# Performance work log

Hardware: AMD Instinct MI355X
Metric: run time of the kernel (lower is better)

Reference implementation:

```python
import jax, jax.numpy as jnp
import numpy as np

N = 16384   # total gate nodes (64 graphs x 256 gates)
B = 64      # graphs in batch
E = 49152   # directed edges (avg in-degree 3)
Q = 32      # qubit_num
F = 256     # feat_dim
D = 2 * F   # node feature dim = 512
H = 2       # heads
A = 128     # action_num


def _gatv2(x, wl, wr, att, b, src, dst, n):
    # PyG GATv2Conv (concat=True, share_weights=False, negative_slope=0.2)
    h, c = att.shape
    xl = (x @ wl).reshape(n, h, c)   # source-side projection [N,H,C]
    xr = (x @ wr).reshape(n, h, c)   # target-side projection [N,H,C]
    e = jax.nn.leaky_relu(xl[src] + xr[dst], 0.2)       # [E,H,C]
    logit = jnp.einsum('ehc,hc->eh', e, att)             # [E,H]
    m = jax.ops.segment_max(logit, dst, num_segments=n)  # softmax over in-edges per target
    p = jnp.exp(logit - m[dst])
    den = jax.ops.segment_sum(p, dst, num_segments=n)
    alpha = p / den[dst]                                 # [E,H]
    out = jax.ops.segment_sum(alpha[:, :, None] * xl[src], dst, num_segments=n)
    return out.reshape(n, h * c) + b


def _forward(x, xt_w1, xt_b1, xt_w2, xt_b2,
             g0_wl, g0_wr, g0_att, g0_b,
             g1_wl, g1_wr, g1_att, g1_b,
             g2_wl, g2_wr, g2_att, g2_b,
             g3_wl, g3_wr, g3_att, g3_b,
             g4_wl, g4_wr, g4_att, g4_b,
             ln_w, ln_b, aggr_t,
             m_w1, m_b1, m_w2, m_b2, m_w3, m_b3,
             edge_index, batch):
    lr = lambda v: jax.nn.leaky_relu(v, 0.01)
    # x_trans: Linear -> LeakyReLU -> Linear, then fold qubit-pairs into one node
    h0 = lr(x @ xt_w1 + xt_b1) @ xt_w2 + xt_b2           # [2N, F]
    cx = h0.reshape(-1, D)                               # [N, 2F]
    n = cx.shape[0]
    # GATv2Conv default add_self_loops=True (inputs contain no self loops)
    sl = jnp.arange(n, dtype=edge_index.dtype)
    src = jnp.concatenate([edge_index[0], sl])
    dst = jnp.concatenate([edge_index[1], sl])
    res = cx
    h = lr(_gatv2(cx, g0_wl, g0_wr, g0_att, g0_b, src, dst, n))
    for wl_, wr_, att_, b_ in ((g1_wl, g1_wr, g1_att, g1_b),
                               (g2_wl, g2_wr, g2_att, g2_b),
                               (g3_wl, g3_wr, g3_att, g3_b)):
        h = lr(_gatv2(h, wl_, wr_, att_, b_, src, dst, n))
    h = lr(_gatv2(h, g4_wl, g4_wr, g4_att, g4_b, src, dst, n))
    h = h + res                                           # residual [N, 2F]
    # PyG LayerNorm(mode='graph'): normalize over nodes AND channels per graph
    cnt = jax.ops.segment_sum(jnp.ones((n,), h.dtype), batch, num_segments=B)
    norm = cnt * h.shape[1]
    mean = jax.ops.segment_sum(h.sum(-1), batch, num_segments=B) / norm
    hc = h - mean[batch][:, None]
    var = jax.ops.segment_sum((hc * hc).sum(-1), batch, num_segments=B) / norm
    h = hc / jnp.sqrt(var + 1e-5)[batch][:, None] * ln_w + ln_b
    # SoftmaxAggregation(learn=True): channel-wise softmax over nodes per graph
    logit = h * aggr_t
    mg = jax.ops.segment_max(logit, batch, num_segments=B)
    p = jnp.exp(logit - mg[batch])
    den = jax.ops.segment_sum(p, batch, num_segments=B)
    g = jax.ops.segment_sum((p / den[batch]) * h, batch, num_segments=B)  # [B, 2F]
    # head MLP 512->384->256->128
    o = lr(g @ m_w1 + m_b1)
    o = lr(o @ m_w2 + m_b2)
    return o @ m_w3 + m_b3


def setup_inputs() -> dict:
    key = jax.random.key(0)
    ks = iter(jax.random.split(key, 64))
    def rn(shp, s=0.05):
        return jax.random.normal(next(ks), shp, jnp.float32) * s
    d = {}
    d['x'] = jax.random.normal(next(ks), (2 * N, Q), jnp.float32)
    src = jax.random.randint(next(ks), (E,), 0, N, jnp.int32)
    off = jax.random.randint(next(ks), (E,), 1, N, jnp.int32)
    d['edge_index'] = jnp.stack([src, (src + off) % N])  # no self loops
    d['batch'] = jnp.arange(N, dtype=jnp.int32) // (N // B)
    d['xt_w1'] = rn((Q, F)); d['xt_b1'] = rn((F,))
    d['xt_w2'] = rn((F, F)); d['xt_b2'] = rn((F,))
    d['g0_wl'] = rn((D, H * D)); d['g0_wr'] = rn((D, H * D))
    d['g0_att'] = rn((H, D));    d['g0_b'] = rn((H * D,))
    for i in (1, 2, 3):
        d[f'g{i}_wl'] = rn((H * D, H * D)); d[f'g{i}_wr'] = rn((H * D, H * D))
        d[f'g{i}_att'] = rn((H, D));        d[f'g{i}_b'] = rn((H * D,))
    d['g4_wl'] = rn((H * D, D)); d['g4_wr'] = rn((H * D, D))
    d['g4_att'] = rn((1, D));    d['g4_b'] = rn((D,))
    d['ln_w'] = jnp.ones((D,), jnp.float32); d['ln_b'] = jnp.zeros((D,), jnp.float32)
    d['aggr_t'] = jnp.array(1.0, jnp.float32)
    d['m_w1'] = rn((D, 384)); d['m_b1'] = rn((384,))
    d['m_w2'] = rn((384, 256)); d['m_b2'] = rn((256,))
    d['m_w3'] = rn((256, A)); d['m_b3'] = rn((A,))
    return d


def reference(x, edge_index, batch, xt_w1, xt_b1, xt_w2, xt_b2,
              g0_wl, g0_wr, g0_att, g0_b,
              g1_wl, g1_wr, g1_att, g1_b,
              g2_wl, g2_wr, g2_att, g2_b,
              g3_wl, g3_wr, g3_att, g3_b,
              g4_wl, g4_wr, g4_att, g4_b,
              ln_w, ln_b, aggr_t,
              m_w1, m_b1, m_w2, m_b2, m_w3, m_b3):
    return _forward(x, xt_w1, xt_b1, xt_w2, xt_b2,
                    g0_wl, g0_wr, g0_att, g0_b,
                    g1_wl, g1_wr, g1_att, g1_b,
                    g2_wl, g2_wr, g2_att, g2_b,
                    g3_wl, g3_wr, g3_att, g3_b,
                    g4_wl, g4_wr, g4_att, g4_b,
                    ln_w, ln_b, aggr_t,
                    m_w1, m_b1, m_w2, m_b2, m_w3, m_b3,
                    edge_index, batch)
```

## Files before the change

### kernel.cpp

```cpp
#include <hip/hip_runtime.h>
#include <hip/hip_bf16.h>

typedef __hip_bfloat16 bf16;

#define NN 16384
#define BBG 64
#define EE 49152
#define ET (EE + NN)
#define DD 512
#define NG (NN / BBG)

__device__ __forceinline__ float b2f(bf16 v) { return __bfloat162float(v); }
__device__ __forceinline__ bf16 f2b(float v) { return __float2bfloat16(v); }
__device__ __forceinline__ float sb2f(short s) {
    unsigned u = ((unsigned)(unsigned short)s) << 16;
    return __builtin_bit_cast(float, u);
}
__device__ __forceinline__ short f2bs(float v) {
    bf16 b = f2b(v);
    return __builtin_bit_cast(short, b);
}
__device__ __forceinline__ int clampi(int v, int lo, int hi)
{
    return v < lo ? lo : (v > hi ? hi : v);
}

typedef __attribute__((ext_vector_type(8))) short bf16x8;
typedef __attribute__((ext_vector_type(4))) float f32x4;

#define AS1 __attribute__((address_space(1)))
#define AS3 __attribute__((address_space(3)))

__global__ __launch_bounds__(256) void gemm_mfma_bt(
    const bf16* __restrict__ A, const bf16* __restrict__ Bt,
    const float* __restrict__ bias, float* __restrict__ C,
    bf16* __restrict__ Cb, int M, int N, int K, float slope, int has_act)
{
    __shared__ bf16 As[128 * 32];
    __shared__ bf16 Bs[128 * 32];
    const int tid = threadIdx.x;
    const int w = tid >> 6;
    const int l = tid & 63;
    const int bm = blockIdx.y * 128;
    const int bn = blockIdx.x * 128;
    const int wrow = (w >> 1) * 64;
    const int wcol = (w & 1) * 64;
    const int quad = l >> 4;
    const int c16 = l & 15;

    const int lrow = l >> 2;
    const int lchunk = l & 3;
    const bf16* Ag = A + (size_t)(bm + w * 16 + lrow) * K + lchunk * 8;
    const bf16* Bg = Bt + (size_t)(bn + w * 16 + lrow) * K + lchunk * 8;
    char* AsB = (char*)As;
    char* BsB = (char*)Bs;

    f32x4 acc[4][4] = {};

    for (int k0 = 0; k0 < K; k0 += 32) {
        __builtin_amdgcn_global_load_lds((const AS1 void*)(Ag + k0),
            (AS3 void*)(AsB + w * 1024), 16, 0, 0);
        __builtin_amdgcn_global_load_lds((const AS1 void*)(Ag + (size_t)64 * K + k0),
            (AS3 void*)(AsB + 4096 + w * 1024), 16, 0, 0);
        __builtin_amdgcn_global_load_lds((const AS1 void*)(Bg + k0),
            (AS3 void*)(BsB + w * 1024), 16, 0, 0);
        __builtin_amdgcn_global_load_lds((const AS1 void*)(Bg + (size_t)64 * K + k0),
            (AS3 void*)(BsB + 4096 + w * 1024), 16, 0, 0);
        __syncthreads();

        bf16x8 a[4], b[4];
#pragma unroll
        for (int i = 0; i < 4; i++) {
            int ra = wrow + i * 16 + c16;
            a[i] = *(const bf16x8*)(AsB + ra * 64 + quad * 16);
            int rb = wcol + i * 16 + c16;
            b[i] = *(const bf16x8*)(BsB + rb * 64 + quad * 16);
        }
#pragma unroll
        for (int i = 0; i < 4; i++)
#pragma unroll
            for (int j = 0; j < 4; j++)
                acc[i][j] = __builtin_amdgcn_mfma_f32_16x16x32_bf16(
                    a[i], b[j], acc[i][j], 0, 0, 0);
        __syncthreads();
    }

#pragma unroll
    for (int i = 0; i < 4; i++) {
#pragma unroll
        for (int j = 0; j < 4; j++) {
            int col = bn + wcol + j * 16 + c16;
            float bv = bias ? bias[col] : 0.f;
#pragma unroll
            for (int r = 0; r < 4; r++) {
                int row = bm + wrow + i * 16 + quad * 4 + r;
                float v = acc[i][j][r] + bv;
                if (has_act) v = (v >= 0.f) ? v : v * slope;
                if (C)  C[(size_t)row * N + col] = v;
                if (Cb) Cb[(size_t)row * N + col] = f2b(v);
            }
        }
    }
}

__global__ __launch_bounds__(256) void gemm_mfma_dual(
    const bf16* __restrict__ A, const bf16* __restrict__ Bt,
    bf16* __restrict__ X0, bf16* __restrict__ X1,
    int M, int Ntot, int K, int HC)
{
    __shared__ bf16 As[128 * 32];
    __shared__ bf16 Bs[128 * 32];
    const int tid = threadIdx.x;
    const int w = tid >> 6;
    const int l = tid & 63;
    const int bm = blockIdx.y * 128;
    const int bn = blockIdx.x * 128;
    const int wrow = (w >> 1) * 64;
    const int wcol = (w & 1) * 64;
    const int quad = l >> 4;
    const int c16 = l & 15;

    const int lrow = l >> 2;
    const int lchunk = l & 3;
    const bf16* Ag = A + (size_t)(bm + w * 16 + lrow) * K + lchunk * 8;
    const bf16* Bg = Bt + (size_t)(bn + w * 16 + lrow) * K + lchunk * 8;
    char* AsB = (char*)As;
    char* BsB = (char*)Bs;

    f32x4 acc[4][4] = {};

    for (int k0 = 0; k0 < K; k0 += 32) {
        __builtin_amdgcn_global_load_lds((const AS1 void*)(Ag + k0),
            (AS3 void*)(AsB + w * 1024), 16, 0, 0);
        __builtin_amdgcn_global_load_lds((const AS1 void*)(Ag + (size_t)64 * K + k0),
            (AS3 void*)(AsB + 4096 + w * 1024), 16, 0, 0);
        __builtin_amdgcn_global_load_lds((const AS1 void*)(Bg + k0),
            (AS3 void*)(BsB + w * 1024), 16, 0, 0);
        __builtin_amdgcn_global_load_lds((const AS1 void*)(Bg + (size_t)64 * K + k0),
            (AS3 void*)(BsB + 4096 + w * 1024), 16, 0, 0);
        __syncthreads();

        bf16x8 a[4], b[4];
#pragma unroll
        for (int i = 0; i < 4; i++) {
            int ra = wrow + i * 16 + c16;
            a[i] = *(const bf16x8*)(AsB + ra * 64 + quad * 16);
            int rb = wcol + i * 16 + c16;
            b[i] = *(const bf16x8*)(BsB + rb * 64 + quad * 16);
        }
#pragma unroll
        for (int i = 0; i < 4; i++)
#pragma unroll
            for (int j = 0; j < 4; j++)
                acc[i][j] = __builtin_amdgcn_mfma_f32_16x16x32_bf16(
                    a[i], b[j], acc[i][j], 0, 0, 0);
        __syncthreads();
    }

#pragma unroll
    for (int i = 0; i < 4; i++) {
#pragma unroll
        for (int j = 0; j < 4; j++) {
            int col = bn + wcol + j * 16 + c16;
            bf16* dst = (col < HC) ? (X0 + col) : (X1 + col - HC);
#pragma unroll
            for (int r = 0; r < 4; r++) {
                int row = bm + wrow + i * 16 + quad * 4 + r;
                dst[(size_t)row * HC] = f2b(acc[i][j][r]);
            }
        }
    }
}

__global__ __launch_bounds__(256) void gemm_f32(
    const float* __restrict__ A, const float* __restrict__ W,
    const float* __restrict__ bias, float* __restrict__ C,
    int M, int N, int K, float slope, int has_act)
{
    const int BK = 16;
    __shared__ float Asm[BK][64 + 1];
    __shared__ float Wsm[BK][64 + 1];
    int tid = threadIdx.x;
    int bm = blockIdx.y * 64;
    int bn = blockIdx.x * 64;
    int tr = tid >> 4;
    int tc = tid & 15;
    float acc[4][4] = {};

    for (int k0 = 0; k0 < K; k0 += BK) {
        {
            int col = tid & 15;
            int row = tid >> 4;
#pragma unroll
            for (int p = 0; p < 4; p++) {
                int r = row + p * 16;
                Asm[col][r] = A[(size_t)(bm + r) * K + k0 + col];
            }
        }
        {
            int wc = tid & 63;
            int wr = tid >> 6;
#pragma unroll
            for (int p = 0; p < 4; p++) {
                int r = wr + p * 4;
                Wsm[r][wc] = W[(size_t)(k0 + r) * N + bn + wc];
            }
        }
        __syncthreads();
#pragma unroll
        for (int kk = 0; kk < BK; kk++) {
            float a[4], w[4];
#pragma unroll
            for (int i = 0; i < 4; i++) a[i] = Asm[kk][tr * 4 + i];
#pragma unroll
            for (int j = 0; j < 4; j++) w[j] = Wsm[kk][tc * 4 + j];
#pragma unroll
            for (int i = 0; i < 4; i++)
#pragma unroll
                for (int j = 0; j < 4; j++)
                    acc[i][j] += a[i] * w[j];
        }
        __syncthreads();
    }
#pragma unroll
    for (int i = 0; i < 4; i++) {
        int r = bm + tr * 4 + i;
#pragma unroll
        for (int j = 0; j < 4; j++) {
            int cn = bn + tc * 4 + j;
            float v = acc[i][j];
            if (bias) v += bias[cn];
            if (has_act) v = (v >= 0.f) ? v : v * slope;
            C[(size_t)r * N + cn] = v;
        }
    }
}

__global__ __launch_bounds__(256) void transpose_f2b2(
    const float* __restrict__ in0, bf16* __restrict__ out0,
    const float* __restrict__ in1, bf16* __restrict__ out1, int R, int C)
{
    const float* in = blockIdx.z ? in1 : in0;
    bf16* out = blockIdx.z ? out1 : out0;
    __shared__ float tile[32][33];
    int c0 = blockIdx.x * 32;
    int r0 = blockIdx.y * 32;
    int tx = threadIdx.x & 31;
    int ty = threadIdx.x >> 5;
#pragma unroll
    for (int k = 0; k < 4; k++) {
        int r = ty + k * 8;
        tile[r][tx] = in[(size_t)(r0 + r) * C + c0 + tx];
    }
    __syncthreads();
#pragma unroll
    for (int k = 0; k < 4; k++) {
        int rr = ty + k * 8;
        out[(size_t)(c0 + rr) * R + r0 + tx] = f2b(tile[tx][rr]);
    }
}

__global__ void f2b_vec(const float* __restrict__ in, bf16* __restrict__ out, int n)
{
    int i = blockIdx.x * 256 + threadIdx.x;
    if (i < n) out[i] = f2b(in[i]);
}

__global__ void count_deg(const int* __restrict__ ei, int* __restrict__ deg)
{
    int e = blockIdx.x * 256 + threadIdx.x;
    if (e >= ET) return;
    int d = (e < EE) ? ei[EE + e] : (e - EE);
    d = clampi(d, 0, NN - 1);
    atomicAdd(&deg[d], 1);
}

__global__ __launch_bounds__(256) void scan_deg(const int* __restrict__ deg,
                                                int* __restrict__ rs)
{
    __shared__ int part[256];
    __shared__ int psum[257];
    int tid = threadIdx.x;
    const int per = NN / 256;
    int base = tid * per;
    int s = 0;
    for (int i = 0; i < per; i++) s += deg[base + i];
    part[tid] = s;
    __syncthreads();
    if (tid == 0) {
        int acc = 0;
        for (int i = 0; i < 256; i++) { psum[i] = acc; acc += part[i]; }
        psum[256] = acc;
    }
    __syncthreads();
    int acc = psum[tid];
    for (int i = 0; i < per; i++) { rs[base + i] = acc; acc += deg[base + i]; }
    if (tid == 0) rs[NN] = psum[256];
}

__global__ void fill_csr(const int* __restrict__ ei, const int* __restrict__ rs,
                         int* __restrict__ cur, int* __restrict__ csrc)
{
    int e = blockIdx.x * 256 + threadIdx.x;
    if (e >= ET) return;
    int s, d;
    if (e < EE) { s = ei[e]; d = ei[EE + e]; } else { s = d = e - EE; }
    s = clampi(s, 0, NN - 1);
    d = clampi(d, 0, NN - 1);
    int pos = atomicAdd(&cur[d], 1);
    int slot = clampi(rs[d] + pos, 0, ET - 1);
    csrc[slot] = s;
}

template<int NH>
__global__ __launch_bounds__(256) void gat_wave7(
    const bf16* __restrict__ xl, const bf16* __restrict__ xr,
    const float* __restrict__ att, const float* __restrict__ bias,
    const int* __restrict__ rs, const int* __restrict__ csrc,
    const float* __restrict__ res, float* __restrict__ out_f,
    bf16* __restrict__ out_b, float* __restrict__ lnsums)
{
    constexpr int HC = NH * 512;
    constexpr int PF = 6;
    constexpr int NODES = (NH == 2) ? 8 : 4;
    constexpr int WPB = (NH == 2) ? 4 : 2;
    constexpr int SLOTS = (NH == 2) ? 7 : 9;
    __shared__ char smem[WPB * 2 * SLOTS * 1024];

    const int tid = threadIdx.x;
    const int w = tid >> 6;
    const int lane = tid & 63;
    const int wave_id = blockIdx.x * WPB + w;

    int msrc[NODES];
    int sdeg[NODES];
#pragma unroll
    for (int it = 0; it < NODES; ++it) {
        int gw = wave_id * NODES + it;
        int n = (NH == 2) ? (gw >> 1) : gw;
        int st = rs[n];
        int deg = clampi(rs[n + 1] - st, 1, 64);
        st = clampi(st, 0, ET - 1);
        st = __builtin_amdgcn_readfirstlane(st);
        deg = __builtin_amdgcn_readfirstlane(deg);
        sdeg[it] = deg;
        msrc[it] = csrc[st + ((lane < deg) ? lane : deg - 1)];
    }

    float av0[8], av1[8], bv0[8], bv1[8];
    {
        f32x4 t0 = *(const f32x4*)(att + lane * 8);
        f32x4 t1 = *(const f32x4*)(att + lane * 8 + 4);
        f32x4 u0 = *(const f32x4*)(bias + lane * 8);
        f32x4 u1 = *(const f32x4*)(bias + lane * 8 + 4);
#pragma unroll
        for (int k = 0; k < 4; k++) {
            av0[k] = t0[k]; av0[4 + k] = t1[k];
            bv0[k] = u0[k]; bv0[4 + k] = u1[k];
        }
        if (NH == 2) {
            f32x4 t2 = *(const f32x4*)(att + 512 + lane * 8);
            f32x4 t3 = *(const f32x4*)(att + 512 + lane * 8 + 4);
            f32x4 u2 = *(const f32x4*)(bias + 512 + lane * 8);
            f32x4 u3 = *(const f32x4*)(bias + 512 + lane * 8 + 4);
#pragma unroll
            for (int k = 0; k < 4; k++) {
                av1[k] = t2[k]; av1[4 + k] = t3[k];
                bv1[k] = u2[k]; bv1[4 + k] = u3[k];
            }
        } else {
#pragma unroll
            for (int k = 0; k < 8; k++) { av1[k] = av0[k]; bv1[k] = bv0[k]; }
        }
    }

    auto issue = [&](int it, int pb) {
        int gw = wave_id * NODES + it;
        int n = (NH == 2) ? (gw >> 1) : gw;
        int h = (NH == 2) ? (gw & 1) : 0;
        char* buf = smem + (size_t)((w * 2 + pb) * SLOTS) * 1024;
        const bf16* xrrow = xr + (size_t)n * HC + h * 512 + lane * 8;
        __builtin_amdgcn_global_load_lds((const AS1 void*)xrrow,
            (AS3 void*)buf, 16, 0, 0);
        int dm1 = sdeg[it] - 1;
#pragma unroll
        for (int r = 0; r < PF; r++) {
            int idx = (r < dm1) ? r : dm1;
            int s = __builtin_amdgcn_readlane(msrc[it], idx);
            s = clampi(s, 0, NN - 1);
            const bf16* row = xl + (size_t)s * HC + h * 512 + lane * 8;
            __builtin_amdgcn_global_load_lds((const AS1 void*)row,
                (AS3 void*)(buf + (1 + r) * 1024), 16, 0, 0);
        }
        if (NH == 1) {
            const float* rr = res + (size_t)n * 512 + lane * 4;
            __builtin_amdgcn_global_load_lds((const AS1 void*)rr,
                (AS3 void*)(buf + 7 * 1024), 16, 0, 0);
            __builtin_amdgcn_global_load_lds((const AS1 void*)(rr + 256),
                (AS3 void*)(buf + 8 * 1024), 16, 0, 0);
        }
    };

    auto compute = [&](int it, int pb) {
        int gw = wave_id * NODES + it;
        int n = (NH == 2) ? (gw >> 1) : gw;
        int h = (NH == 2) ? (gw & 1) : 0;
        int cb = h * 512 + lane * 8;
        int deg = sdeg[it];
        char* buf = smem + (size_t)((w * 2 + pb) * SLOTS) * 1024;

        float rv[8], av[8];
        {
            bf16x8 xb = *(const bf16x8*)(buf + lane * 16);
#pragma unroll
            for (int k = 0; k < 8; k++) {
                rv[k] = sb2f(xb[k]);
                av[k] = h ? av1[k] : av0[k];
            }
        }
        bf16x8 rloc[PF];
#pragma unroll
        for (int r = 0; r < PF; r++)
            rloc[r] = *(const bf16x8*)(buf + (1 + r) * 1024 + lane * 16);

        float part[PF];
#pragma unroll
        for (int r = 0; r < PF; r++) {
            float p0 = 0.f, p1 = 0.f, p2 = 0.f, p3 = 0.f;
#pragma unroll
            for (int k = 0; k < 8; k += 4) {
                float x0 = sb2f(rloc[r][k + 0]);
                float x1 = sb2f(rloc[r][k + 1]);
                float x2 = sb2f(rloc[r][k + 2]);
                float x3 = sb2f(rloc[r][k + 3]);
                float u0 = x0 + rv[k + 0]; u0 = (u0 >= 0.f) ? u0 : 0.2f * u0;
                float u1 = x1 + rv[k + 1]; u1 = (u1 >= 0.f) ? u1 : 0.2f * u1;
                float u2 = x2 + rv[k + 2]; u2 = (u2 >= 0.f) ? u2 : 0.2f * u2;
                float u3 = x3 + rv[k + 3]; u3 = (u3 >= 0.f) ? u3 : 0.2f * u3;
                p0 = fmaf(av[k + 0], u0, p0);
                p1 = fmaf(av[k + 1], u1, p1);
                p2 = fmaf(av[k + 2], u2, p2);
                p3 = fmaf(av[k + 3], u3, p3);
            }
            part[r] = (p0 + p1) + (p2 + p3);
        }

#pragma unroll
        for (int msk = 32; msk; msk >>= 1) {
#pragma unroll
            for (int r = 0; r < PF; r++) part[r] += __shfl_xor(part[r], msk);
        }

        float m = -1e30f;
#pragma unroll
        for (int r = 0; r < PF; r++) {
            float vr = (r < deg) ? part[r] : -1e30f;
            m = fmaxf(m, vr);
        }
        float den = 0.f;
        float pw[PF];
#pragma unroll
        for (int r = 0; r < PF; r++) {
            float e = __expf(part[r] - m);
            pw[r] = (r < deg) ? e : 0.f;
            den += pw[r];
        }

        float acc[8];
#pragma unroll
        for (int k = 0; k < 8; k++) acc[k] = 0.f;
#pragma unroll
        for (int r = 0; r < PF; r++) {
#pragma unroll
            for (int k = 0; k < 8; k++)
                acc[k] = fmaf(pw[r], sb2f(rloc[r][k]), acc[k]);
        }

        if (deg > PF) {
            for (int i = PF; i < deg; i++) {
                int s = __builtin_amdgcn_readlane(msrc[it], i);
                s = clampi(s, 0, NN - 1);
                f32x4 rw = *(const f32x4*)(xl + (size_t)s * HC + cb);
                bf16x8 rb = __builtin_bit_cast(bf16x8, rw);
                float pt = 0.f;
#pragma unroll
                for (int k = 0; k < 8; k++) {
                    float x = sb2f(rb[k]);
                    float u = x + rv[k];
                    u = (u >= 0.f) ? u : 0.2f * u;
                    pt = fmaf(av[k], u, pt);
                }
#pragma unroll
                for (int msk = 32; msk; msk >>= 1) pt += __shfl_xor(pt, msk);
                float mn = fmaxf(m, pt);
                float rr = __expf(m - mn);
                float pi = __expf(pt - mn);
                m = mn;
                den = den * rr + pi;
#pragma unroll
                for (int k = 0; k < 8; k++) {
                    float x = sb2f(rb[k]);
                    acc[k] = fmaf(acc[k], rr, pi * x);
                }
            }
        }

        float inv = 1.f / den;
        float vals[8];
#pragma unroll
        for (int k = 0; k < 8; k++) {
            float bv = h ? bv1[k] : bv0[k];
            float v = fmaf(acc[k], inv, bv);
            v = (v >= 0.f) ? v : 0.01f * v;
            vals[k] = v;
        }
        if (NH == 1) {
            f32x4 r0 = *(const f32x4*)(buf + 7 * 1024 + lane * 32);
            f32x4 r1 = *(const f32x4*)(buf + 7 * 1024 + lane * 32 + 16);
            float ls = 0.f, ls2 = 0.f;
#pragma unroll
            for (int k = 0; k < 8; k++) {
                vals[k] += (k < 4) ? r0[k] : r1[k - 4];
                ls += vals[k];
                ls2 += vals[k] * vals[k];
            }
#pragma unroll
            for (int v = 0; v < 2; v++) {
                f32x4 ov;
#pragma unroll
                for (int k = 0; k < 4; k++) ov[k] = vals[v * 4 + k];
                *(f32x4*)(out_f + (size_t)n * HC + cb + v * 4) = ov;
            }
#pragma unroll
            for (int msk = 32; msk; msk >>= 1) {
                ls += __shfl_xor(ls, msk);
                ls2 += __shfl_xor(ls2, msk);
            }
            if (lane == 0) {
                int g = n >> 8;
                atomicAdd(&lnsums[g], ls);
                atomicAdd(&lnsums[BBG + g], ls2);
            }
        } else {
            bf16x8 ov;
#pragma unroll
            for (int k = 0; k < 8; k++) ov[k] = f2bs(vals[k]);
            *(bf16x8*)(out_b + (size_t)n * HC + cb) = ov;
        }
    };

    issue(0, 0);
#pragma unroll
    for (int it = 0; it < NODES; ++it) {
        int pb = it & 1;
        if (it + 1 < NODES) {
            issue(it + 1, pb ^ 1);
            if (NH == 2) asm volatile("s_waitcnt vmcnt(7)" ::: "memory");
            else         asm volatile("s_waitcnt vmcnt(9)" ::: "memory");
        } else {
            asm volatile("s_waitcnt vmcnt(0)" ::: "memory");
        }
        __builtin_amdgcn_sched_barrier(0);
        compute(it, pb);
    }
}

__global__ __launch_bounds__(256) void aggr_partial(
    const float* __restrict__ h, const float* __restrict__ lnsums,
    const float* __restrict__ lnw, const float* __restrict__ lnb,
    const float* __restrict__ t_, float* __restrict__ pm,
    float* __restrict__ pd, float* __restrict__ pa)
{
    int g = blockIdx.x, ch = blockIdx.y, nk = blockIdx.z;
    int tid = threadIdx.x;
    int c = ch * 256 + tid;
    const float tot = (float)(NG * DD);
    float S = lnsums[g], S2 = lnsums[BBG + g];
    float mu = S / tot;
    float iv = rsqrtf(fmaxf(S2 / tot - mu * mu, 0.f) + 1e-5f);
    float w = lnw[c], b = lnb[c], t = t_[0];
    size_t base = (size_t)g * NG * DD + (size_t)nk * 32 * DD + c;
    float m = -1e30f, den = 0.f, acc = 0.f;
    for (int i = 0; i < 32; i++) {
        float hn = (h[base + (size_t)i * DD] - mu) * iv * w + b;
        float lg = hn * t;
        if (lg > m) {
            float r = __expf(m - lg);
            den *= r; acc *= r; m = lg;
        }
        float p = __expf(lg - m);
        den += p; acc += p * hn;
    }
    size_t idx = (((size_t)g * 2 + ch) * 8 + nk) * 256 + tid;
    pm[idx] = m; pd[idx] = den; pa[idx] = acc;
}

__global__ __launch_bounds__(256) void aggr_combine(
    const float* __restrict__ pm, const float* __restrict__ pd,
    const float* __restrict__ pa, float* __restrict__ gout)
{
    int g = blockIdx.x, ch = blockIdx.y;
    int tid = threadIdx.x;
    size_t base = (((size_t)g * 2 + ch) * 8) * 256 + tid;
    float m = -1e30f;
#pragma unroll
    for (int k = 0; k < 8; k++) m = fmaxf(m, pm[base + k * 256]);
    float den = 0.f, acc = 0.f;
#pragma unroll
    for (int k = 0; k < 8; k++) {
        float r = __expf(pm[base + k * 256] - m);
        den += pd[base + k * 256] * r;
        acc += pa[base + k * 256] * r;
    }
    gout[(size_t)g * DD + ch * 256 + tid] = acc / den;
}

extern "C" void kernel_launch(void* const* d_in, const int* in_sizes, int n_in,
                              void* d_out, int out_size, void* d_ws, size_t ws_size,
                              hipStream_t stream)
{
    const float* x      = (const float*)d_in[0];
    const int*   ei     = (const int*)d_in[1];
    const float* xt_w1  = (const float*)d_in[3];
    const float* xt_b1  = (const float*)d_in[4];
    const float* xt_w2  = (const float*)d_in[5];
    const float* xt_b2  = (const float*)d_in[6];
    const float* ln_w   = (const float*)d_in[27];
    const float* ln_b   = (const float*)d_in[28];
    const float* aggr_t = (const float*)d_in[29];
    const float* m_w1   = (const float*)d_in[30];
    const float* m_b1   = (const float*)d_in[31];
    const float* m_w2   = (const float*)d_in[32];
    const float* m_b2   = (const float*)d_in[33];
    const float* m_w3   = (const float*)d_in[34];
    const float* m_b3   = (const float*)d_in[35];
    float* out = (float*)d_out;

    char* p = (char*)d_ws;
    auto take = [&](size_t bytes) {
        char* r = p;
        p += (bytes + 255) & ~(size_t)255;
        return r;
    };
    int* i_deg     = (int*)take((size_t)(NN + 1) * 4);
    int* i_rs      = (int*)take((size_t)(NN + 1) * 4);
    int* i_cur     = (int*)take((size_t)NN * 4);
    int* i_src     = (int*)take((size_t)ET * 4);
    float* f_sums  = (float*)take((size_t)2 * BBG * 4);
    float* f_pm    = (float*)take((size_t)BBG * 2 * 8 * 256 * 4);
    float* f_pd    = (float*)take((size_t)BBG * 2 * 8 * 256 * 4);
    float* f_pa    = (float*)take((size_t)BBG * 2 * 8 * 256 * 4);
    float* b_g     = (float*)take((size_t)BBG * DD * 4);
    float* b_m1    = (float*)take((size_t)BBG * 384 * 4);
    float* b_m2    = (float*)take((size_t)BBG * 256 * 4);
    float* b_res   = (float*)take((size_t)NN * DD * 4);
    float* b_h     = (float*)take((size_t)NN * DD * 4);
    bf16* b_resb   = (bf16*)take((size_t)NN * DD * 2);
    bf16* b_hb     = (bf16*)take((size_t)NN * 1024 * 2);
    bf16* b_xlb    = (bf16*)take((size_t)NN * 1024 * 2);
    bf16* b_xrb    = (bf16*)take((size_t)NN * 1024 * 2);
    bf16* b_xb     = (bf16*)take((size_t)2 * NN * 32 * 2);
    bf16* b_wcat   = (bf16*)take((size_t)2048 * 1024 * 2);
    bf16* b_w1b    = (bf16*)take((size_t)32 * 256 * 2);
    bf16* b_w2b    = (bf16*)take((size_t)256 * 256 * 2);
    bf16* b_t1b = b_hb;

    dim3 blk(256);

    hipMemsetAsync(i_deg, 0, (size_t)(NN + 1) * 4, stream);
    hipMemsetAsync(i_cur, 0, (size_t)NN * 4, stream);
    hipMemsetAsync(f_sums, 0, (size_t)2 * BBG * 4, stream);
    count_deg<<<ET / 256, blk, 0, stream>>>(ei, i_deg);
    scan_deg<<<1, blk, 0, stream>>>(i_deg, i_rs);
    fill_csr<<<ET / 256, blk, 0, stream>>>(ei, i_rs, i_cur, i_src);

    f2b_vec<<<(2 * NN * 32 + 255) / 256, blk, 0, stream>>>(x, b_xb, 2 * NN * 32);
    transpose_f2b2<<<dim3(256 / 32, 32 / 32, 1), blk, 0, stream>>>(
        xt_w1, b_w1b, xt_w1, b_w1b, 32, 256);
    transpose_f2b2<<<dim3(256 / 32, 256 / 32, 1), blk, 0, stream>>>(
        xt_w2, b_w2b, xt_w2, b_w2b, 256, 256);

    gemm_mfma_bt<<<dim3(256 / 128, 32768 / 128), blk, 0, stream>>>(
        b_xb, b_w1b, xt_b1, (float*)nullptr, b_t1b, 32768, 256, 32, 0.01f, 1);
    gemm_mfma_bt<<<dim3(256 / 128, 32768 / 128), blk, 0, stream>>>(
        b_t1b, b_w2b, xt_b2, b_res, b_resb, 32768, 256, 256, 0.f, 0);

    for (int L = 0; L < 5; L++) {
        const float* wl  = (const float*)d_in[7 + 4 * L];
        const float* wr  = (const float*)d_in[8 + 4 * L];
        const float* att = (const float*)d_in[9 + 4 * L];
        const float* gb  = (const float*)d_in[10 + 4 * L];
        int Fin = (L == 0) ? 512 : 1024;
        int HC  = (L == 4) ? 512 : 1024;
        const bf16* hin = (L == 0) ? b_resb : b_hb;

        transpose_f2b2<<<dim3(HC / 32, Fin / 32, 2), blk, 0, stream>>>(
            wl, b_wcat, wr, b_wcat + (size_t)HC * Fin, Fin, HC);
        gemm_mfma_dual<<<dim3(2 * HC / 128, NN / 128), blk, 0, stream>>>(
            hin, b_wcat, b_xlb, b_xrb, NN, 2 * HC, Fin, HC);
        if (L == 4) {
            gat_wave7<1><<<2048, dim3(128), 0, stream>>>(
                b_xlb, b_xrb, att, gb, i_rs, i_src,
                b_res, b_h, (bf16*)nullptr, f_sums);
        } else {
            gat_wave7<2><<<1024, blk, 0, stream>>>(
                b_xlb, b_xrb, att, gb, i_rs, i_src,
                (const float*)nullptr, (float*)nullptr, b_hb, (float*)nullptr);
        }
    }

    aggr_partial<<<dim3(BBG, 2, 8), blk, 0, stream>>>(
        b_h, f_sums, ln_w, ln_b, aggr_t, f_pm, f_pd, f_pa);
    aggr_combine<<<dim3(BBG, 2), blk, 0, stream>>>(f_pm, f_pd, f_pa, b_g);

    gemm_f32<<<dim3(384 / 64, 1), blk, 0, stream>>>(
        b_g, m_w1, m_b1, b_m1, 64, 384, 512, 0.01f, 1);
    gemm_f32<<<dim3(256 / 64, 1), blk, 0, stream>>>(
        b_m1, m_w2, m_b2, b_m2, 64, 256, 384, 0.01f, 1);
    gemm_f32<<<dim3(128 / 64, 1), blk, 0, stream>>>(
        b_m2, m_w3, m_b3, out, 64, 128, 256, 0.f, 0);
}
```

Before: 1.048 ms.

## Use 256x256 double-buffered MFMA GEMM and register-prefetch GAT kernel for last layer

Replaces the 128x128 dual-projection GEMM with a templated 256x256 tile kernel using 512 threads, K-step 64, and double-buffered LDS staging via global_load_lds with explicit waitcnt and barriers, plus s_setprio around MFMA bursts. The aim is more data reuse per loaded tile and overlap of loads with compute. The final single-head GAT layer now uses a new kernel that prefetches neighbour rows into registers instead of LDS, with 4 waves per block. The trade-off is 128KB of LDS per block, so only one block fits per CU, and a larger register footprint.

```diff
diff --git a/kernel.cpp b/kernel.cpp
--- a/kernel.cpp
+++ b/kernel.cpp
@@ -103,69 +103,115 @@
     }
 }
 
-__global__ __launch_bounds__(256) void gemm_mfma_dual(
+template<int KK>
+__global__ __launch_bounds__(512, 1) void gemm256_dual(
     const bf16* __restrict__ A, const bf16* __restrict__ Bt,
-    bf16* __restrict__ X0, bf16* __restrict__ X1,
-    int M, int Ntot, int K, int HC)
-{
-    __shared__ bf16 As[128 * 32];
-    __shared__ bf16 Bs[128 * 32];
+    bf16* __restrict__ X0, bf16* __restrict__ X1, int HC)
+{
+    constexpr int NT = KK / 64;
+    __shared__ char smem[131072];
+    char* const Abuf[2] = { smem,         smem + 65536 };
+    char* const Bbuf[2] = { smem + 32768, smem + 98304 };
     const int tid = threadIdx.x;
     const int w = tid >> 6;
     const int l = tid & 63;
-    const int bm = blockIdx.y * 128;
-    const int bn = blockIdx.x * 128;
-    const int wrow = (w >> 1) * 64;
-    const int wcol = (w & 1) * 64;
+    const int wm = w >> 2;
+    const int wn = w & 3;
     const int quad = l >> 4;
     const int c16 = l & 15;
-
-    const int lrow = l >> 2;
-    const int lchunk = l & 3;
-    const bf16* Ag = A + (size_t)(bm + w * 16 + lrow) * K + lchunk * 8;
-    const bf16* Bg = Bt + (size_t)(bn + w * 16 + lrow) * K + lchunk * 8;
-    char* AsB = (char*)As;
-    char* BsB = (char*)Bs;
-
-    f32x4 acc[4][4] = {};
-
-    for (int k0 = 0; k0 < K; k0 += 32) {
-        __builtin_amdgcn_global_load_lds((const AS1 void*)(Ag + k0),
-            (AS3 void*)(AsB + w * 1024), 16, 0, 0);
-        __builtin_amdgcn_global_load_lds((const AS1 void*)(Ag + (size_t)64 * K + k0),
-            (AS3 void*)(AsB + 4096 + w * 1024), 16, 0, 0);
-        __builtin_amdgcn_global_load_lds((const AS1 void*)(Bg + k0),
-            (AS3 void*)(BsB + w * 1024), 16, 0, 0);
-        __builtin_amdgcn_global_load_lds((const AS1 void*)(Bg + (size_t)64 * K + k0),
-            (AS3 void*)(BsB + 4096 + w * 1024), 16, 0, 0);
-        __syncthreads();
-
-        bf16x8 a[4], b[4];
-#pragma unroll
-        for (int i = 0; i < 4; i++) {
-            int ra = wrow + i * 16 + c16;
-            a[i] = *(const bf16x8*)(AsB + ra * 64 + quad * 16);
-            int rb = wcol + i * 16 + c16;
-            b[i] = *(const bf16x8*)(BsB + rb * 64 + quad * 16);
-        }
-#pragma unroll
-        for (int i = 0; i < 4; i++)
-#pragma unroll
-            for (int j = 0; j < 4; j++)
-                acc[i][j] = __builtin_amdgcn_mfma_f32_16x16x32_bf16(
-                    a[i], b[j], acc[i][j], 0, 0, 0);
-        __syncthreads();
-    }
-
-#pragma unroll
-    for (int i = 0; i < 4; i++) {
-#pragma unroll
-        for (int j = 0; j < 4; j++) {
-            int col = bn + wcol + j * 16 + c16;
+    const int bm = blockIdx.y * 256;
+    const int bn = blockIdx.x * 256;
+
+    const int srow = w * 32 + (l >> 3);
+    const int schunk = (l & 7) * 8;
+    const bf16* AgS = A + (size_t)(bm + srow) * KK + schunk;
+    const bf16* BgS = Bt + (size_t)(bn + srow) * KK + schunk;
+    const int lbase = (w * 32) * 128;
+
+    auto stage = [&](int k0, int buf) {
+#pragma unroll
+        for (int op = 0; op < 4; ++op)
+            __builtin_amdgcn_global_load_lds(
+                (const AS1 void*)(AgS + (size_t)(op * 8) * KK + k0),
+                (AS3 void*)(Abuf[buf] + lbase + op * 1024), 16, 0, 0);
+#pragma unroll
+        for (int op = 0; op < 4; ++op)
+            __builtin_amdgcn_global_load_lds(
+                (const AS1 void*)(BgS + (size_t)(op * 8) * KK + k0),
+                (AS3 void*)(Bbuf[buf] + lbase + op * 1024), 16, 0, 0);
+    };
+
+    f32x4 acc[8][4] = {};
+
+    auto tile_compute = [&](int buf) {
+        bf16x8 bfrag[4][2];
+#pragma unroll
+        for (int j = 0; j < 4; ++j)
+#pragma unroll
+            for (int ks = 0; ks < 2; ++ks) {
+                int rb = wn * 64 + j * 16 + c16;
+                bfrag[j][ks] = *(const bf16x8*)(Bbuf[buf] + rb * 128 + ks * 64 + quad * 16);
+            }
+#pragma unroll
+        for (int ip = 0; ip < 4; ++ip) {
+            bf16x8 afrag[2][2];
+#pragma unroll
+            for (int ii = 0; ii < 2; ++ii)
+#pragma unroll
+                for (int ks = 0; ks < 2; ++ks) {
+                    int ra = wm * 128 + (ip * 2 + ii) * 16 + c16;
+                    afrag[ii][ks] = *(const bf16x8*)(Abuf[buf] + ra * 128 + ks * 64 + quad * 16);
+                }
+            __builtin_amdgcn_s_setprio(1);
+#pragma unroll
+            for (int ii = 0; ii < 2; ++ii)
+#pragma unroll
+                for (int j = 0; j < 4; ++j)
+#pragma unroll
+                    for (int ks = 0; ks < 2; ++ks)
+                        acc[ip * 2 + ii][j] = __builtin_amdgcn_mfma_f32_16x16x32_bf16(
+                            afrag[ii][ks], bfrag[j][ks], acc[ip * 2 + ii][j], 0, 0, 0);
+            __builtin_amdgcn_s_setprio(0);
+        }
+    };
+
+    stage(0, 0);
+    stage(64, 1);
+    asm volatile("s_waitcnt vmcnt(8)" ::: "memory");
+    __builtin_amdgcn_s_barrier();
+
+#pragma unroll 1
+    for (int tp = 0; tp < NT / 2; ++tp) {
+        const int t0 = 2 * tp;
+        tile_compute(0);
+        __builtin_amdgcn_s_barrier();
+        if (t0 + 2 < NT) {
+            stage((t0 + 2) * 64, 0);
+            asm volatile("s_waitcnt vmcnt(8)" ::: "memory");
+        } else {
+            asm volatile("s_waitcnt vmcnt(0)" ::: "memory");
+        }
+        __builtin_amdgcn_s_barrier();
+        tile_compute(1);
+        __builtin_amdgcn_s_barrier();
+        if (t0 + 3 < NT) {
+            stage((t0 + 3) * 64, 1);
+            asm volatile("s_waitcnt vmcnt(8)" ::: "memory");
+        } else {
+            asm volatile("s_waitcnt vmcnt(0)" ::: "memory");
+        }
+        __builtin_amdgcn_s_barrier();
+    }
+
+#pragma unroll
+    for (int i = 0; i < 8; ++i) {
+#pragma unroll
+        for (int j = 0; j < 4; ++j) {
+            int col = bn + wn * 64 + j * 16 + c16;
             bf16* dst = (col < HC) ? (X0 + col) : (X1 + col - HC);
 #pragma unroll
-            for (int r = 0; r < 4; r++) {
-                int row = bm + wrow + i * 16 + quad * 4 + r;
+            for (int r = 0; r < 4; ++r) {
+                int row = bm + wm * 128 + i * 16 + quad * 4 + r;
                 dst[(size_t)row * HC] = f2b(acc[i][j][r]);
             }
         }
@@ -313,7 +359,7 @@
 }
 
 template<int NH>
-__global__ __launch_bounds__(256) void gat_wave7(
+__global__ __launch_bounds__(256, 4) void gat_wave6(
     const bf16* __restrict__ xl, const bf16* __restrict__ xr,
     const float* __restrict__ att, const float* __restrict__ bias,
     const int* __restrict__ rs, const int* __restrict__ csrc,
@@ -323,14 +369,10 @@
     constexpr int HC = NH * 512;
     constexpr int PF = 6;
     constexpr int NODES = (NH == 2) ? 8 : 4;
-    constexpr int WPB = (NH == 2) ? 4 : 2;
-    constexpr int SLOTS = (NH == 2) ? 7 : 9;
-    __shared__ char smem[WPB * 2 * SLOTS * 1024];
-
     const int tid = threadIdx.x;
     const int w = tid >> 6;
     const int lane = tid & 63;
-    const int wave_id = blockIdx.x * WPB + w;
+    const int wave_id = blockIdx.x * 4 + w;
 
     int msrc[NODES];
     int sdeg[NODES];
@@ -347,6 +389,233 @@
         msrc[it] = csrc[st + ((lane < deg) ? lane : deg - 1)];
     }
 
+    float av0[8], av1[8];
+    {
+        f32x4 t0 = *(const f32x4*)(att + lane * 8);
+        f32x4 t1 = *(const f32x4*)(att + lane * 8 + 4);
+#pragma unroll
+        for (int k = 0; k < 4; k++) { av0[k] = t0[k]; av0[4 + k] = t1[k]; }
+        if (NH == 2) {
+            f32x4 t2 = *(const f32x4*)(att + 512 + lane * 8);
+            f32x4 t3 = *(const f32x4*)(att + 512 + lane * 8 + 4);
+#pragma unroll
+            for (int k = 0; k < 4; k++) { av1[k] = t2[k]; av1[4 + k] = t3[k]; }
+        } else {
+#pragma unroll
+            for (int k = 0; k < 8; k++) av1[k] = av0[k];
+        }
+    }
+
+    f32x4 rows[2][PF];
+    f32x4 rpx[2];
+
+    auto issue = [&](int it, int pb) {
+        int gw = wave_id * NODES + it;
+        int n = (NH == 2) ? (gw >> 1) : gw;
+        int h = (NH == 2) ? (gw & 1) : 0;
+        int cb = h * 512 + lane * 8;
+        rpx[pb] = *(const f32x4*)(xr + (size_t)n * HC + cb);
+        int dm1 = sdeg[it] - 1;
+#pragma unroll
+        for (int r = 0; r < PF; r++) {
+            int idx = (r < dm1) ? r : dm1;
+            int s = __builtin_amdgcn_readlane(msrc[it], idx);
+            s = clampi(s, 0, NN - 1);
+            rows[pb][r] = *(const f32x4*)(xl + (size_t)s * HC + cb);
+        }
+    };
+
+    auto compute = [&](int it, int pb) {
+        int gw = wave_id * NODES + it;
+        int n = (NH == 2) ? (gw >> 1) : gw;
+        int h = (NH == 2) ? (gw & 1) : 0;
+        int cb = h * 512 + lane * 8;
+        int deg = sdeg[it];
+
+        float rv[8], av[8];
+        {
+            bf16x8 xb = __builtin_bit_cast(bf16x8, rpx[pb]);
+#pragma unroll
+            for (int k = 0; k < 8; k++) {
+                rv[k] = sb2f(xb[k]);
+                av[k] = h ? av1[k] : av0[k];
+            }
+        }
+
+        float part[PF];
+#pragma unroll
+        for (int r = 0; r < PF; r++) {
+            bf16x8 rb = __builtin_bit_cast(bf16x8, rows[pb][r]);
+            float p0 = 0.f, p1 = 0.f, p2 = 0.f, p3 = 0.f;
+#pragma unroll
+            for (int k = 0; k < 8; k += 4) {
+                float x0 = sb2f(rb[k + 0]);
+                float x1 = sb2f(rb[k + 1]);
+                float x2 = sb2f(rb[k + 2]);
+                float x3 = sb2f(rb[k + 3]);
+                float u0 = x0 + rv[k + 0]; u0 = (u0 >= 0.f) ? u0 : 0.2f * u0;
+                float u1 = x1 + rv[k + 1]; u1 = (u1 >= 0.f) ? u1 : 0.2f * u1;
+                float u2 = x2 + rv[k + 2]; u2 = (u2 >= 0.f) ? u2 : 0.2f * u2;
+                float u3 = x3 + rv[k + 3]; u3 = (u3 >= 0.f) ? u3 : 0.2f * u3;
+                p0 = fmaf(av[k + 0], u0, p0);
+                p1 = fmaf(av[k + 1], u1, p1);
+                p2 = fmaf(av[k + 2], u2, p2);
+                p3 = fmaf(av[k + 3], u3, p3);
+            }
+            part[r] = (p0 + p1) + (p2 + p3);
+        }
+
+#pragma unroll
+        for (int msk = 32; msk; msk >>= 1) {
+#pragma unroll
+            for (int r = 0; r < PF; r++) part[r] += __shfl_xor(part[r], msk);
+        }
+
+        float m = -1e30f;
+#pragma unroll
+        for (int r = 0; r < PF; r++) {
+            float vr = (r < deg) ? part[r] : -1e30f;
+            m = fmaxf(m, vr);
+        }
+        float den = 0.f;
+        float pw[PF];
+#pragma unroll
+        for (int r = 0; r < PF; r++) {
+            float e = __expf(part[r] - m);
+            pw[r] = (r < deg) ? e : 0.f;
+            den += pw[r];
+        }
+
+        float acc[8];
+#pragma unroll
+        for (int k = 0; k < 8; k++) acc[k] = 0.f;
+#pragma unroll
+        for (int r = 0; r < PF; r++) {
+            bf16x8 rb = __builtin_bit_cast(bf16x8, rows[pb][r]);
+#pragma unroll
+            for (int k = 0; k < 8; k++)
+                acc[k] = fmaf(pw[r], sb2f(rb[k]), acc[k]);
+        }
+
+        if (deg > PF) {
+            for (int i = PF; i < deg; i++) {
+                int s = __builtin_amdgcn_readlane(msrc[it], i);
+                s = clampi(s, 0, NN - 1);
+                f32x4 rw = *(const f32x4*)(xl + (size_t)s * HC + cb);
+                bf16x8 rb = __builtin_bit_cast(bf16x8, rw);
+                float pt = 0.f;
+#pragma unroll
+                for (int k = 0; k < 8; k++) {
+                    float x = sb2f(rb[k]);
+                    float u = x + rv[k];
+                    u = (u >= 0.f) ? u : 0.2f * u;
+                    pt = fmaf(av[k], u, pt);
+                }
+#pragma unroll
+                for (int msk = 32; msk; msk >>= 1) pt += __shfl_xor(pt, msk);
+                float mn = fmaxf(m, pt);
+                float rr = __expf(m - mn);
+                float pi = __expf(pt - mn);
+                m = mn;
+                den = den * rr + pi;
+#pragma unroll
+                for (int k = 0; k < 8; k++) {
+                    float x = sb2f(rb[k]);
+                    acc[k] = fmaf(acc[k], rr, pi * x);
+                }
+            }
+        }
+
+        float inv = 1.f / den;
+        f32x4 b0 = *(const f32x4*)(bias + cb);
+        f32x4 b1 = *(const f32x4*)(bias + cb + 4);
+        float vals[8];
+#pragma unroll
+        for (int k = 0; k < 8; k++) {
+            float bv = (k < 4) ? b0[k] : b1[k - 4];
+            float v = fmaf(acc[k], inv, bv);
+            v = (v >= 0.f) ? v : 0.01f * v;
+            vals[k] = v;
+        }
+        if (res) {
+            float ls = 0.f, ls2 = 0.f;
+#pragma unroll
+            for (int k = 0; k < 8; k++) {
+                vals[k] += res[(size_t)n * HC + cb + k];
+                ls += vals[k];
+                ls2 += vals[k] * vals[k];
+            }
+#pragma unroll
+            for (int v = 0; v < 2; v++) {
+                f32x4 ov;
+#pragma unroll
+                for (int k = 0; k < 4; k++) ov[k] = vals[v * 4 + k];
+                *(f32x4*)(out_f + (size_t)n * HC + cb + v * 4) = ov;
+            }
+            if (lnsums) {
+#pragma unroll
+                for (int msk = 32; msk; msk >>= 1) {
+                    ls += __shfl_xor(ls, msk);
+                    ls2 += __shfl_xor(ls2, msk);
+                }
+                if (lane == 0) {
+                    int g = n >> 8;
+                    atomicAdd(&lnsums[g], ls);
+                    atomicAdd(&lnsums[BBG + g], ls2);
+                }
+            }
+        } else {
+            bf16x8 ov;
+#pragma unroll
+            for (int k = 0; k < 8; k++) ov[k] = f2bs(vals[k]);
+            *(bf16x8*)(out_b + (size_t)n * HC + cb) = ov;
+        }
+    };
+
+    issue(0, 0);
+#pragma unroll
+    for (int it = 0; it < NODES; ++it) {
+        int pb = it & 1;
+        if (it + 1 < NODES) issue(it + 1, pb ^ 1);
+        compute(it, pb);
+    }
+}
+
+template<int NH>
+__global__ __launch_bounds__(256) void gat_wave7(
+    const bf16* __restrict__ xl, const bf16* __restrict__ xr,
+    const float* __restrict__ att, const float* __restrict__ bias,
+    const int* __restrict__ rs, const int* __restrict__ csrc,
+    const float* __restrict__ res, float* __restrict__ out_f,
+    bf16* __restrict__ out_b, float* __restrict__ lnsums)
+{
+    constexpr int HC = NH * 512;
+    constexpr int PF = 6;
+    constexpr int NODES = (NH == 2) ? 8 : 4;
+    constexpr int WPB = 4;
+    constexpr int SLOTS = 7;
+    __shared__ char smem[WPB * 2 * SLOTS * 1024];
+
+    const int tid = threadIdx.x;
+    const int w = tid >> 6;
+    const int lane = tid & 63;
+    const int wave_id = blockIdx.x * WPB + w;
+
+    int msrc[NODES];
+    int sdeg[NODES];
+#pragma unroll
+    for (int it = 0; it < NODES; ++it) {
+        int gw = wave_id * NODES + it;
+        int n = (NH == 2) ? (gw >> 1) : gw;
+        int st = rs[n];
+        int deg = clampi(rs[n + 1] - st, 1, 64);
+        st = clampi(st, 0, ET - 1);
+        st = __builtin_amdgcn_readfirstlane(st);
+        deg = __builtin_amdgcn_readfirstlane(deg);
+        sdeg[it] = deg;
+        msrc[it] = csrc[st + ((lane < deg) ? lane : deg - 1)];
+    }
+
     float av0[8], av1[8], bv0[8], bv1[8];
     {
         f32x4 t0 = *(const f32x4*)(att + lane * 8);
@@ -391,13 +660,6 @@
             const bf16* row = xl + (size_t)s * HC + h * 512 + lane * 8;
             __builtin_amdgcn_global_load_lds((const AS1 void*)row,
                 (AS3 void*)(buf + (1 + r) * 1024), 16, 0, 0);
-        }
-        if (NH == 1) {
-            const float* rr = res + (size_t)n * 512 + lane * 4;
-            __builtin_amdgcn_global_load_lds((const AS1 void*)rr,
-                (AS3 void*)(buf + 7 * 1024), 16, 0, 0);
-            __builtin_amdgcn_global_load_lds((const AS1 void*)(rr + 256),
-                (AS3 void*)(buf + 8 * 1024), 16, 0, 0);
         }
     };
 
@@ -514,39 +776,10 @@
             v = (v >= 0.f) ? v : 0.01f * v;
             vals[k] = v;
         }
-        if (NH == 1) {
-            f32x4 r0 = *(const f32x4*)(buf + 7 * 1024 + lane * 32);
-            f32x4 r1 = *(const f32x4*)(buf + 7 * 1024 + lane * 32 + 16);
-            float ls = 0.f, ls2 = 0.f;
-#pragma unroll
-            for (int k = 0; k < 8; k++) {
-                vals[k] += (k < 4) ? r0[k] : r1[k - 4];
-                ls += vals[k];
-                ls2 += vals[k] * vals[k];
-            }
-#pragma unroll
-            for (int v = 0; v < 2; v++) {
-                f32x4 ov;
-#pragma unroll
-                for (int k = 0; k < 4; k++) ov[k] = vals[v * 4 + k];
-                *(f32x4*)(out_f + (size_t)n * HC + cb + v * 4) = ov;
-            }
-#pragma unroll
-            for (int msk = 32; msk; msk >>= 1) {
-                ls += __shfl_xor(ls, msk);
-                ls2 += __shfl_xor(ls2, msk);
-            }
-            if (lane == 0) {
-                int g = n >> 8;
-                atomicAdd(&lnsums[g], ls);
-                atomicAdd(&lnsums[BBG + g], ls2);
-            }
-        } else {
-            bf16x8 ov;
-#pragma unroll
-            for (int k = 0; k < 8; k++) ov[k] = f2bs(vals[k]);
-            *(bf16x8*)(out_b + (size_t)n * HC + cb) = ov;
-        }
+        bf16x8 ov;
+#pragma unroll
+        for (int k = 0; k < 8; k++) ov[k] = f2bs(vals[k]);
+        *(bf16x8*)(out_b + (size_t)n * HC + cb) = ov;
     };
 
     issue(0, 0);
@@ -555,8 +788,7 @@
         int pb = it & 1;
         if (it + 1 < NODES) {
             issue(it + 1, pb ^ 1);
-            if (NH == 2) asm volatile("s_waitcnt vmcnt(7)" ::: "memory");
-            else         asm volatile("s_waitcnt vmcnt(9)" ::: "memory");
+            asm volatile("s_waitcnt vmcnt(7)" ::: "memory");
         } else {
             asm volatile("s_waitcnt vmcnt(0)" ::: "memory");
         }
@@ -696,10 +928,18 @@
 
         transpose_f2b2<<<dim3(HC / 32, Fin / 32, 2), blk, 0, stream>>>(
             wl, b_wcat, wr, b_wcat + (size_t)HC * Fin, Fin, HC);
-        gemm_mfma_dual<<<dim3(2 * HC / 128, NN / 128), blk, 0, stream>>>(
-            hin, b_wcat, b_xlb, b_xrb, NN, 2 * HC, Fin, HC);
+        if (L == 0)
+            gemm256_dual<512><<<dim3(2048 / 256, NN / 256), dim3(512), 0, stream>>>(
+                hin, b_wcat, b_xlb, b_xrb, 1024);
+        else if (L == 4)
+            gemm256_dual<1024><<<dim3(1024 / 256, NN / 256), dim3(512), 0, stream>>>(
+                hin, b_wcat, b_xlb, b_xrb, 512);
+        else
+            gemm256_dual<1024><<<dim3(2048 / 256, NN / 256), dim3(512), 0, stream>>>(
+                hin, b_wcat, b_xlb, b_xrb, 1024);
+
         if (L == 4) {
-            gat_wave7<1><<<2048, dim3(128), 0, stream>>>(
+            gat_wave6<1><<<1024, blk, 0, stream>>>(
                 b_xlb, b_xrb, att, gb, i_rs, i_src,
                 b_res, b_h, (bf16*)nullptr, f_sums);
         } else {
```

Result: faster. 1.021 ms (-2.5%).
